# Performance work log

Measured on AMD Instinct MI355X. Metric: run time of the kernel, lower is better.

## Reference

```python
import jax, jax.numpy as jnp
import numpy as np

N_NODES = 50000
N_EDGES = 640000
N_SUPPORT = 3
D_IN = 128
D_OUT = 128


def setup_inputs() -> dict:
    key = jax.random.key(0)
    k = jax.random.split(key, 6)
    x = jax.random.normal(k[0], (N_NODES, D_IN), dtype=jnp.float32)
    edge_rows = jax.random.randint(k[1], (N_SUPPORT, N_EDGES), 0, N_NODES, dtype=jnp.int32)
    edge_cols = jax.random.randint(k[2], (N_SUPPORT, N_EDGES), 0, N_NODES, dtype=jnp.int32)
    edge_vals = jax.random.uniform(k[3], (N_SUPPORT, N_EDGES), dtype=jnp.float32)
    weights = jax.random.normal(k[4], (N_SUPPORT, D_IN, D_OUT), dtype=jnp.float32) * 0.05
    bias = jax.random.normal(k[5], (D_OUT,), dtype=jnp.float32) * 0.01
    return {"x": x, "edge_rows": edge_rows, "edge_cols": edge_cols,
            "edge_vals": edge_vals, "weights": weights, "bias": bias}


def reference(x, edge_rows, edge_cols, edge_vals, weights, bias):
    # Dense projection per support: [S, N, D_OUT]
    pre = jnp.einsum('nd,sdo->sno', x, weights)

    def spmm(rows, cols, vals, dense):
        # sparse [N,N] @ dense [N,D] via gather + scatter-add
        msgs = vals[:, None] * dense[cols]          # [E, D]
        return jax.ops.segment_sum(msgs, rows, num_segments=dense.shape[0])

    out = jax.vmap(spmm)(edge_rows, edge_cols, edge_vals, pre).sum(axis=0)
    return jax.nn.relu(out + bias)
```

## Files before the change

### kernel.cpp

```cpp
#include <hip/hip_runtime.h>

#define N_NODES 50000
#define N_EDGES 640000
#define N_SUP   3
#define D       128
#define NTOT    150000
#define E_TOT   1920000
#define NC      293
#define CAPC    7680
#define CAPB    9216
#define CTILE   2048
#define CTPS    313
#define SBLKS   (N_SUP * CTPS)
#define XCBLKS  3125
#define WBLKS   96
#define LDSTR   132

typedef __attribute__((ext_vector_type(2))) float f32x2;
typedef __attribute__((ext_vector_type(4))) float f32x4;
typedef __attribute__((ext_vector_type(8))) short s16x8;

__device__ __forceinline__ unsigned short f2bf(float f) {
    unsigned int u = __float_as_uint(f);
    u += 0x7FFFu + ((u >> 16) & 1u);
    return (unsigned short)(u >> 16);
}

__global__ __launch_bounds__(512) void prep_scatter(
    const int* __restrict__ rows, const int* __restrict__ cols,
    const float* __restrict__ vals, int* __restrict__ coarse_wptr,
    uint2* __restrict__ sortedA,
    const float4* __restrict__ x, ushort4* __restrict__ xb,
    const float* __restrict__ W, unsigned short* __restrict__ Wf)
{
    int tid = threadIdx.x;

    if (blockIdx.x >= SBLKS) {
        int gid = (blockIdx.x - SBLKS) * 512 + tid;
        if (gid < N_NODES * D / 4) {
            float4 v = x[gid];
            ushort4 o;
            o.x = f2bf(v.x); o.y = f2bf(v.y); o.z = f2bf(v.z); o.w = f2bf(v.w);
            xb[gid] = o;
        } else {
            int g2 = gid - N_NODES * D / 4;
            if (g2 < N_SUP * D * D) {
                int j    = g2 & 7;
                int lane = (g2 >> 3) & 63;
                int rest = g2 >> 9;
                int nt = rest & 7, kb = (rest >> 3) & 3, s = rest >> 5;
                int k = kb * 32 + ((lane >> 4) * 8) + j;
                int n = nt * 16 + (lane & 15);
                Wf[g2] = f2bf(W[((size_t)s * D + k) * D + n]);
            }
        }
        return;
    }

    __shared__ int          h[512];
    __shared__ int          toff[512];
    __shared__ int          gbase[512];
    __shared__ uint2        stage[CTILE];
    __shared__ unsigned int dst[CTILE];

    h[tid] = 0;
    __syncthreads();

    int s  = blockIdx.x / CTPS;
    int tb = (blockIdx.x % CTPS) * CTILE;
    int n  = N_EDGES - tb; if (n > CTILE) n = CTILE;
    const int*   rp = rows + (size_t)s * N_EDGES + tb;
    const int*   cp = cols + (size_t)s * N_EDGES + tb;
    const float* vp = vals + (size_t)s * N_EDGES + tb;

    int bk[4], rk[4]; uint2 ed[4];
    #pragma unroll
    for (int i = 0; i < 4; ++i) {
        int idx = tid + i * 512;
        bk[i] = -1;
        if (idx < n) {
            int grow = s * N_NODES + rp[idx];
            bk[i] = grow >> 9;
            rk[i] = atomicAdd(&h[bk[i]], 1);
            ed[i] = make_uint2(((unsigned int)(grow & 511) << 16)
                               | (unsigned int)cp[idx],
                               __float_as_uint(vp[idx]));
        }
    }
    __syncthreads();
    int cntb = h[tid];
    __syncthreads();
    for (int off = 1; off < 512; off <<= 1) {
        int t = (tid >= off) ? h[tid - off] : 0;
        __syncthreads();
        h[tid] += t;
        __syncthreads();
    }
    toff[tid]  = h[tid] - cntb;
    gbase[tid] = (cntb > 0) ? atomicAdd(&coarse_wptr[tid], cntb) : 0;
    __syncthreads();

    #pragma unroll
    for (int i = 0; i < 4; ++i) {
        if (bk[i] >= 0) {
            int slot = toff[bk[i]] + rk[i];
            int gslot = gbase[bk[i]] + rk[i];
            stage[slot] = ed[i];
            dst[slot] = (gslot < CAPC)
                      ? (unsigned int)(bk[i] * CAPC + gslot)
                      : 0xFFFFFFFFu;
        }
    }
    __syncthreads();
    for (int j = tid; j < n; j += 512) {
        unsigned int d = dst[j];
        if (d != 0xFFFFFFFFu) sortedA[d] = stage[j];
    }
}

__global__ __launch_bounds__(512) void bucket_sort(
    const int* __restrict__ coarse_wptr, const uint2* __restrict__ sortedA,
    int* __restrict__ row_ptr2, unsigned int* __restrict__ sortedB)
{
    int c  = blockIdx.x;
    int cnt = coarse_wptr[c];
    if (cnt > CAPC) cnt = CAPC;

    __shared__ int hist[512];
    __shared__ int rank[512];
    __shared__ int fin[512];
    int tid = threadIdx.x;
    hist[tid] = 0;

    const uint2* src = sortedA + (size_t)c * CAPC;
    uint2 e[15];
    #pragma unroll
    for (int k = 0; k < 15; ++k) {
        int idx = tid + k * 512;
        if (idx < cnt) e[k] = src[idx];
    }
    __syncthreads();
    #pragma unroll
    for (int k = 0; k < 15; ++k) {
        int idx = tid + k * 512;
        if (idx < cnt) atomicAdd(&hist[e[k].x >> 16], 1);
    }
    __syncthreads();

    int padded = (hist[tid] + 3) & ~3;
    hist[tid] = padded;
    __syncthreads();
    for (int off = 1; off < 512; off <<= 1) {
        int t = (tid >= off) ? hist[tid - off] : 0;
        __syncthreads();
        hist[tid] += t;
        __syncthreads();
    }
    int start = c * CAPB + hist[tid] - padded;
    rank[tid] = start;
    fin [tid] = start + padded;
    row_ptr2[c * 513 + tid] = start;
    if (tid == 511) row_ptr2[c * 513 + 512] = c * CAPB + hist[511];
    __syncthreads();

    #pragma unroll
    for (int k = 0; k < 15; ++k) {
        int idx = tid + k * 512;
        if (idx < cnt) {
            int r = atomicAdd(&rank[e[k].x >> 16], 1);
            sortedB[r] = ((unsigned int)f2bf(__uint_as_float(e[k].y)) << 16)
                       | (e[k].x & 0xFFFFu);
        }
    }
    __syncthreads();
    for (int p = rank[tid]; p < fin[tid]; ++p) sortedB[p] = 0;
}

__global__ __launch_bounds__(256) void gather_gemm(
    const unsigned short* __restrict__ xb, const int* __restrict__ row_ptr2,
    const unsigned int* __restrict__ sortedB,
    const unsigned short* __restrict__ Wf,
    const float* __restrict__ bias, float* __restrict__ out)
{
    __shared__ unsigned short ys[48 * LDSTR];
    __shared__ int rs[48], re[48];
    const int tid  = threadIdx.x;
    const int w    = tid >> 6;
    const int lane = tid & 63;
    const int m0   = blockIdx.x * 16;

    if (tid < 48) {
        int grow = (tid >> 4) * N_NODES + m0 + (tid & 15);
        int rpi  = (grow >> 9) * 513 + (grow & 511);
        rs[tid] = row_ptr2[rpi];
        re[tid] = row_ptr2[rpi + 1];
    }
    __syncthreads();

    const int hh = lane >> 5;
    const int u  = lane & 31;
    for (int r = w; r < 48; r += 4) {
        int start = rs[r], end = re[r];
        f32x2 accA = {0.f, 0.f}, accB = {0.f, 0.f};
        for (int j = start; j < end; j += 64) {
            int m = end - j; if (m > 64) m = 64;
            unsigned int ev = (lane < m) ? sortedB[j + lane] : 0u;
            for (int t = 0; t < m; t += 4) {
                unsigned int e0 = (unsigned int)__shfl((int)ev, t + hh);
                unsigned int e1 = (unsigned int)__shfl((int)ev, t + 2 + hh);
                float v0 = __uint_as_float(e0 & 0xFFFF0000u);
                float v1 = __uint_as_float(e1 & 0xFFFF0000u);
                uint2 X0 = *((const uint2*)(xb + (size_t)(e0 & 0xFFFFu) * D) + u);
                uint2 X1 = *((const uint2*)(xb + (size_t)(e1 & 0xFFFFu) * D) + u);
                f32x2 xa0 = {__uint_as_float(X0.x << 16),
                             __uint_as_float(X0.x & 0xFFFF0000u)};
                f32x2 xb0 = {__uint_as_float(X0.y << 16),
                             __uint_as_float(X0.y & 0xFFFF0000u)};
                f32x2 xa1 = {__uint_as_float(X1.x << 16),
                             __uint_as_float(X1.x & 0xFFFF0000u)};
                f32x2 xb1 = {__uint_as_float(X1.y << 16),
                             __uint_as_float(X1.y & 0xFFFF0000u)};
                accA += v0 * xa0;
                accB += v0 * xb0;
                accA += v1 * xa1;
                accB += v1 * xb1;
            }
        }
        float a0 = accA.x, a1 = accA.y, a2 = accB.x, a3 = accB.y;
        a0 += __shfl_xor(a0, 32);
        a1 += __shfl_xor(a1, 32);
        a2 += __shfl_xor(a2, 32);
        a3 += __shfl_xor(a3, 32);
        if (hh == 0) {
            uint2 o;
            o.x = (unsigned int)f2bf(a0) | ((unsigned int)f2bf(a1) << 16);
            o.y = (unsigned int)f2bf(a2) | ((unsigned int)f2bf(a3) << 16);
            *(uint2*)(ys + r * LDSTR + u * 4) = o;
        }
    }
    __syncthreads();

    const int quad = lane >> 4;
    const int l16  = lane & 15;
    const int nt0  = w * 2;
    f32x4 acc0 = {0.f, 0.f, 0.f, 0.f}, acc1 = {0.f, 0.f, 0.f, 0.f};

    #pragma unroll
    for (int s = 0; s < N_SUP; ++s) {
        #pragma unroll
        for (int kb = 0; kb < 4; ++kb) {
            union { uint2 q[2]; s16x8 v; } A;
            const unsigned short* ap = ys + (s * 16 + l16) * LDSTR
                                          + kb * 32 + quad * 8;
            A.q[0] = *(const uint2*)ap;
            A.q[1] = *(const uint2*)(ap + 4);
            const unsigned short* wf = Wf + (size_t)((s * 4 + kb) * 8 + nt0) * 64 * 8
                                          + lane * 8;
            s16x8 b0 = *(const s16x8*)wf;
            s16x8 b1 = *(const s16x8*)(wf + 64 * 8);
            acc0 = __builtin_amdgcn_mfma_f32_16x16x32_bf16(A.v, b0, acc0, 0, 0, 0);
            acc1 = __builtin_amdgcn_mfma_f32_16x16x32_bf16(A.v, b1, acc1, 0, 0, 0);
        }
    }

    #pragma unroll
    for (int p = 0; p < 2; ++p) {
        int col = (nt0 + p) * 16 + l16;
        float bv = bias[col];
        f32x4 a = p ? acc1 : acc0;
        #pragma unroll
        for (int r = 0; r < 4; ++r) {
            int row = m0 + quad * 4 + r;
            out[(size_t)row * D + col] = fmaxf(a[r] + bv, 0.f);
        }
    }
}

extern "C" void kernel_launch(void* const* d_in, const int* in_sizes, int n_in,
                              void* d_out, int out_size, void* d_ws, size_t ws_size,
                              hipStream_t stream)
{
    const float* x         = (const float*)d_in[0];
    const int*   edge_rows = (const int*)  d_in[1];
    const int*   edge_cols = (const int*)  d_in[2];
    const float* edge_vals = (const float*)d_in[3];
    const float* weights   = (const float*)d_in[4];
    const float* bias      = (const float*)d_in[5];
    float* out = (float*)d_out;

    char* ws = (char*)d_ws;
    size_t off = 0;
    auto alloc = [&](size_t bytes) -> char* {
        char* p = ws + off;
        off += (bytes + 255) & ~(size_t)255;
        return p;
    };
    int*            coarse_wptr = (int*)            alloc(512 * 4);
    int*            row_ptr2    = (int*)            alloc((size_t)NC * 513 * 4);
    unsigned short* xb          = (unsigned short*) alloc((size_t)N_NODES * D * 2);
    unsigned short* Wf          = (unsigned short*) alloc((size_t)N_SUP * D * D * 2);
    uint2*          sortedA     = (uint2*)          alloc((size_t)NC * CAPC * 8);
    unsigned int*   sortedB     = (unsigned int*)   alloc((size_t)NC * CAPB * 4);

    hipMemsetAsync(coarse_wptr, 0, 512 * 4, stream);
    prep_scatter<<<SBLKS + XCBLKS + WBLKS, 512, 0, stream>>>(
        edge_rows, edge_cols, edge_vals, coarse_wptr, sortedA,
        (const float4*)x, (ushort4*)xb, weights, Wf);
    bucket_sort <<<NC, 512, 0, stream>>>(coarse_wptr, sortedA,
                                         row_ptr2, sortedB);
    gather_gemm <<<N_NODES / 16, 256, 0, stream>>>(xb, row_ptr2, sortedB,
                                                   Wf, bias, out);
}
```

Measured before the change: 197.7 us.

## Build CSR with global count, scan and atomic placement instead of bucket sort

Replaces the two-level sort (coarse LDS-staged scatter into buckets, then a per-bucket sort) with three passes. The first counts edges per row with global atomics, fused with the bf16 conversion of x and W. The second scans the counts per 512-row chunk, and the third places each edge directly into its slot with a global atomic on a per-row write pointer. This removes the intermediate sortedA buffer and its write and read traffic. In exchange it issues two global atomics per edge, writes scattered 4-byte entries, and drops the padding of row lengths to multiples of four that the gather kernel may have relied on.

Measured after the change: 378.7 us. 91.6% more time.

```diff
diff --git a/kernel.cpp b/kernel.cpp
--- a/kernel.cpp
+++ b/kernel.cpp
@@ -7,11 +7,8 @@
 #define NTOT    150000
 #define E_TOT   1920000
 #define NC      293
-#define CAPC    7680
 #define CAPB    9216
-#define CTILE   2048
-#define CTPS    313
-#define SBLKS   (N_SUP * CTPS)
+#define CBLKS   938
 #define XCBLKS  3125
 #define WBLKS   96
 #define LDSTR   132
@@ -26,154 +23,93 @@
     return (unsigned short)(u >> 16);
 }
 
-__global__ __launch_bounds__(512) void prep_scatter(
-    const int* __restrict__ rows, const int* __restrict__ cols,
-    const float* __restrict__ vals, int* __restrict__ coarse_wptr,
-    uint2* __restrict__ sortedA,
+__global__ __launch_bounds__(512) void count_convert(
+    const int* __restrict__ rows, int* __restrict__ row_cnt,
     const float4* __restrict__ x, ushort4* __restrict__ xb,
     const float* __restrict__ W, unsigned short* __restrict__ Wf)
 {
     int tid = threadIdx.x;
 
-    if (blockIdx.x >= SBLKS) {
-        int gid = (blockIdx.x - SBLKS) * 512 + tid;
-        if (gid < N_NODES * D / 4) {
-            float4 v = x[gid];
-            ushort4 o;
-            o.x = f2bf(v.x); o.y = f2bf(v.y); o.z = f2bf(v.z); o.w = f2bf(v.w);
-            xb[gid] = o;
-        } else {
-            int g2 = gid - N_NODES * D / 4;
-            if (g2 < N_SUP * D * D) {
-                int j    = g2 & 7;
-                int lane = (g2 >> 3) & 63;
-                int rest = g2 >> 9;
-                int nt = rest & 7, kb = (rest >> 3) & 3, s = rest >> 5;
-                int k = kb * 32 + ((lane >> 4) * 8) + j;
-                int n = nt * 16 + (lane & 15);
-                Wf[g2] = f2bf(W[((size_t)s * D + k) * D + n]);
+    if (blockIdx.x < CBLKS) {
+        int base = blockIdx.x * 2048 + tid;
+        #pragma unroll
+        for (int i = 0; i < 4; ++i) {
+            int idx = base + i * 512;
+            if (idx < E_TOT) {
+                int s = idx / N_EDGES;
+                atomicAdd(&row_cnt[s * N_NODES + rows[idx]], 1);
             }
         }
         return;
     }
 
-    __shared__ int          h[512];
-    __shared__ int          toff[512];
-    __shared__ int          gbase[512];
-    __shared__ uint2        stage[CTILE];
-    __shared__ unsigned int dst[CTILE];
-
-    h[tid] = 0;
+    int gid = (blockIdx.x - CBLKS) * 512 + tid;
+    if (gid < N_NODES * D / 4) {
+        float4 v = x[gid];
+        ushort4 o;
+        o.x = f2bf(v.x); o.y = f2bf(v.y); o.z = f2bf(v.z); o.w = f2bf(v.w);
+        xb[gid] = o;
+    } else {
+        int g2 = gid - N_NODES * D / 4;
+        if (g2 < N_SUP * D * D) {
+            int j    = g2 & 7;
+            int lane = (g2 >> 3) & 63;
+            int rest = g2 >> 9;
+            int nt = rest & 7, kb = (rest >> 3) & 3, s = rest >> 5;
+            int k = kb * 32 + ((lane >> 4) * 8) + j;
+            int n = nt * 16 + (lane & 15);
+            Wf[g2] = f2bf(W[((size_t)s * D + k) * D + n]);
+        }
+    }
+}
+
+__global__ __launch_bounds__(512) void scan_rows(
+    const int* __restrict__ row_cnt, int* __restrict__ row_ptr2,
+    int* __restrict__ row_wptr)
+{
+    __shared__ int wsum[8];
+    int c    = blockIdx.x;
+    int tid  = threadIdx.x;
+    int lane = tid & 63;
+    int w    = tid >> 6;
+    int grow = c * 512 + tid;
+    int cnt  = (grow < NTOT) ? row_cnt[grow] : 0;
+
+    int v = cnt;
+    #pragma unroll
+    for (int d = 1; d < 64; d <<= 1) {
+        int t = __shfl_up(v, d);
+        v += (lane >= d) ? t : 0;
+    }
+    if (lane == 63) wsum[w] = v;
     __syncthreads();
-
-    int s  = blockIdx.x / CTPS;
-    int tb = (blockIdx.x % CTPS) * CTILE;
-    int n  = N_EDGES - tb; if (n > CTILE) n = CTILE;
-    const int*   rp = rows + (size_t)s * N_EDGES + tb;
-    const int*   cp = cols + (size_t)s * N_EDGES + tb;
-    const float* vp = vals + (size_t)s * N_EDGES + tb;
-
-    int bk[4], rk[4]; uint2 ed[4];
+    int base = c * CAPB;
+    #pragma unroll
+    for (int i = 0; i < 8; ++i) base += (i < w) ? wsum[i] : 0;
+
+    int start = base + v - cnt;
+    row_ptr2[c * 513 + tid] = start;
+    if (grow < NTOT) row_wptr[grow] = start;
+    if (tid == 511) row_ptr2[c * 513 + 512] = base + v;
+}
+
+__global__ __launch_bounds__(512) void place(
+    const int* __restrict__ rows, const int* __restrict__ cols,
+    const float* __restrict__ vals, int* __restrict__ row_wptr,
+    unsigned int* __restrict__ sortedB)
+{
+    int base = blockIdx.x * 2048 + threadIdx.x;
     #pragma unroll
     for (int i = 0; i < 4; ++i) {
-        int idx = tid + i * 512;
-        bk[i] = -1;
-        if (idx < n) {
-            int grow = s * N_NODES + rp[idx];
-            bk[i] = grow >> 9;
-            rk[i] = atomicAdd(&h[bk[i]], 1);
-            ed[i] = make_uint2(((unsigned int)(grow & 511) << 16)
-                               | (unsigned int)cp[idx],
-                               __float_as_uint(vp[idx]));
-        }
-    }
-    __syncthreads();
-    int cntb = h[tid];
-    __syncthreads();
-    for (int off = 1; off < 512; off <<= 1) {
-        int t = (tid >= off) ? h[tid - off] : 0;
-        __syncthreads();
-        h[tid] += t;
-        __syncthreads();
-    }
-    toff[tid]  = h[tid] - cntb;
-    gbase[tid] = (cntb > 0) ? atomicAdd(&coarse_wptr[tid], cntb) : 0;
-    __syncthreads();
-
-    #pragma unroll
-    for (int i = 0; i < 4; ++i) {
-        if (bk[i] >= 0) {
-            int slot = toff[bk[i]] + rk[i];
-            int gslot = gbase[bk[i]] + rk[i];
-            stage[slot] = ed[i];
-            dst[slot] = (gslot < CAPC)
-                      ? (unsigned int)(bk[i] * CAPC + gslot)
-                      : 0xFFFFFFFFu;
-        }
-    }
-    __syncthreads();
-    for (int j = tid; j < n; j += 512) {
-        unsigned int d = dst[j];
-        if (d != 0xFFFFFFFFu) sortedA[d] = stage[j];
-    }
-}
-
-__global__ __launch_bounds__(512) void bucket_sort(
-    const int* __restrict__ coarse_wptr, const uint2* __restrict__ sortedA,
-    int* __restrict__ row_ptr2, unsigned int* __restrict__ sortedB)
-{
-    int c  = blockIdx.x;
-    int cnt = coarse_wptr[c];
-    if (cnt > CAPC) cnt = CAPC;
-
-    __shared__ int hist[512];
-    __shared__ int rank[512];
-    __shared__ int fin[512];
-    int tid = threadIdx.x;
-    hist[tid] = 0;
-
-    const uint2* src = sortedA + (size_t)c * CAPC;
-    uint2 e[15];
-    #pragma unroll
-    for (int k = 0; k < 15; ++k) {
-        int idx = tid + k * 512;
-        if (idx < cnt) e[k] = src[idx];
-    }
-    __syncthreads();
-    #pragma unroll
-    for (int k = 0; k < 15; ++k) {
-        int idx = tid + k * 512;
-        if (idx < cnt) atomicAdd(&hist[e[k].x >> 16], 1);
-    }
-    __syncthreads();
-
-    int padded = (hist[tid] + 3) & ~3;
-    hist[tid] = padded;
-    __syncthreads();
-    for (int off = 1; off < 512; off <<= 1) {
-        int t = (tid >= off) ? hist[tid - off] : 0;
-        __syncthreads();
-        hist[tid] += t;
-        __syncthreads();
-    }
-    int start = c * CAPB + hist[tid] - padded;
-    rank[tid] = start;
-    fin [tid] = start + padded;
-    row_ptr2[c * 513 + tid] = start;
-    if (tid == 511) row_ptr2[c * 513 + 512] = c * CAPB + hist[511];
-    __syncthreads();
-
-    #pragma unroll
-    for (int k = 0; k < 15; ++k) {
-        int idx = tid + k * 512;
-        if (idx < cnt) {
-            int r = atomicAdd(&rank[e[k].x >> 16], 1);
-            sortedB[r] = ((unsigned int)f2bf(__uint_as_float(e[k].y)) << 16)
-                       | (e[k].x & 0xFFFFu);
-        }
-    }
-    __syncthreads();
-    for (int p = rank[tid]; p < fin[tid]; ++p) sortedB[p] = 0;
+        int idx = base + i * 512;
+        if (idx < E_TOT) {
+            int s    = idx / N_EDGES;
+            int grow = s * N_NODES + rows[idx];
+            int pos  = atomicAdd(&row_wptr[grow], 1);
+            sortedB[pos] = ((unsigned int)f2bf(vals[idx]) << 16)
+                         | (unsigned int)cols[idx];
+        }
+    }
 }
 
 __global__ __launch_bounds__(256) void gather_gemm(
@@ -295,19 +231,19 @@
         off += (bytes + 255) & ~(size_t)255;
         return p;
     };
-    int*            coarse_wptr = (int*)            alloc(512 * 4);
-    int*            row_ptr2    = (int*)            alloc((size_t)NC * 513 * 4);
-    unsigned short* xb          = (unsigned short*) alloc((size_t)N_NODES * D * 2);
-    unsigned short* Wf          = (unsigned short*) alloc((size_t)N_SUP * D * D * 2);
-    uint2*          sortedA     = (uint2*)          alloc((size_t)NC * CAPC * 8);
-    unsigned int*   sortedB     = (unsigned int*)   alloc((size_t)NC * CAPB * 4);
-
-    hipMemsetAsync(coarse_wptr, 0, 512 * 4, stream);
-    prep_scatter<<<SBLKS + XCBLKS + WBLKS, 512, 0, stream>>>(
-        edge_rows, edge_cols, edge_vals, coarse_wptr, sortedA,
-        (const float4*)x, (ushort4*)xb, weights, Wf);
-    bucket_sort <<<NC, 512, 0, stream>>>(coarse_wptr, sortedA,
-                                         row_ptr2, sortedB);
-    gather_gemm <<<N_NODES / 16, 256, 0, stream>>>(xb, row_ptr2, sortedB,
-                                                   Wf, bias, out);
-}
+    int*            row_cnt  = (int*)            alloc((size_t)NTOT * 4);
+    int*            row_wptr = (int*)            alloc((size_t)NTOT * 4);
+    int*            row_ptr2 = (int*)            alloc((size_t)NC * 513 * 4);
+    unsigned short* xb       = (unsigned short*) alloc((size_t)N_NODES * D * 2);
+    unsigned short* Wf       = (unsigned short*) alloc((size_t)N_SUP * D * D * 2);
+    unsigned int*   sortedB  = (unsigned int*)   alloc((size_t)(NC + 1) * CAPB * 4);
+
+    hipMemsetAsync(row_cnt, 0, (size_t)NTOT * 4, stream);
+    count_convert<<<CBLKS + XCBLKS + WBLKS, 512, 0, stream>>>(
+        edge_rows, row_cnt, (const float4*)x, (ushort4*)xb, weights, Wf);
+    scan_rows<<<NC, 512, 0, stream>>>(row_cnt, row_ptr2, row_wptr);
+    place<<<CBLKS, 512, 0, stream>>>(edge_rows, edge_cols, edge_vals,
+                                     row_wptr, sortedB);
+    gather_gemm<<<N_NODES / 16, 256, 0, stream>>>(xb, row_ptr2, sortedB,
+                                                  Wf, bias, out);
+}
```

## Split edge staging into packed key and bf16 value arrays, use wave-shuffle scans

Applied to the files above, without the earlier changes.

Edges in the intermediate coarse-bucket buffer are now stored as a 4-byte packed row/col key plus a 2-byte bf16 value, instead of an 8-byte uint2 with an fp32 value. The bf16 conversion moves into the first pass, which cuts intermediate write and read bytes. Both LDS Hillis-Steele prefix scans are replaced with a wave-level __shfl_up scan plus a cross-wave sum, removing many __syncthreads. The global bucket counters are spaced 16 ints apart to reduce atomic contention. Per-row padding to a multiple of 4 and its zero-fill are dropped (CAPB becomes CAPC). That is a risk if gather_gemm assumes rows padded to 4 entries.

Result: no change. 199.1 us (+0.7%).

```diff
diff --git a/kernel.cpp b/kernel.cpp
--- a/kernel.cpp
+++ b/kernel.cpp
@@ -8,7 +8,6 @@
 #define E_TOT   1920000
 #define NC      293
 #define CAPC    7680
-#define CAPB    9216
 #define CTILE   2048
 #define CTPS    313
 #define SBLKS   (N_SUP * CTPS)
@@ -29,7 +28,7 @@
 __global__ __launch_bounds__(512) void prep_scatter(
     const int* __restrict__ rows, const int* __restrict__ cols,
     const float* __restrict__ vals, int* __restrict__ coarse_wptr,
-    uint2* __restrict__ sortedA,
+    unsigned int* __restrict__ sortedM, unsigned short* __restrict__ sortedV,
     const float4* __restrict__ x, ushort4* __restrict__ xb,
     const float* __restrict__ W, unsigned short* __restrict__ Wf)
 {
@@ -57,11 +56,16 @@
         return;
     }
 
-    __shared__ int          h[512];
-    __shared__ int          toff[512];
-    __shared__ int          gbase[512];
-    __shared__ uint2        stage[CTILE];
-    __shared__ unsigned int dst[CTILE];
+    __shared__ int            h[512];
+    __shared__ int            toff[512];
+    __shared__ int            gbase[512];
+    __shared__ int            wsum[8];
+    __shared__ unsigned int   stageM[CTILE];
+    __shared__ unsigned short stageV[CTILE];
+    __shared__ unsigned int   dst[CTILE];
+
+    const int lane = tid & 63;
+    const int w    = tid >> 6;
 
     h[tid] = 0;
     __syncthreads();
@@ -73,7 +77,7 @@
     const int*   cp = cols + (size_t)s * N_EDGES + tb;
     const float* vp = vals + (size_t)s * N_EDGES + tb;
 
-    int bk[4], rk[4]; uint2 ed[4];
+    int bk[4], rk[4]; unsigned int edM[4]; unsigned short edV[4];
     #pragma unroll
     for (int i = 0; i < 4; ++i) {
         int idx = tid + i * 512;
@@ -82,30 +86,37 @@
             int grow = s * N_NODES + rp[idx];
             bk[i] = grow >> 9;
             rk[i] = atomicAdd(&h[bk[i]], 1);
-            ed[i] = make_uint2(((unsigned int)(grow & 511) << 16)
-                               | (unsigned int)cp[idx],
-                               __float_as_uint(vp[idx]));
+            edM[i] = ((unsigned int)(grow & 511) << 16) | (unsigned int)cp[idx];
+            edV[i] = f2bf(vp[idx]);
         }
     }
     __syncthreads();
     int cntb = h[tid];
-    __syncthreads();
-    for (int off = 1; off < 512; off <<= 1) {
-        int t = (tid >= off) ? h[tid - off] : 0;
-        __syncthreads();
-        h[tid] += t;
-        __syncthreads();
-    }
-    toff[tid]  = h[tid] - cntb;
-    gbase[tid] = (cntb > 0) ? atomicAdd(&coarse_wptr[tid], cntb) : 0;
+
+    int v = cntb;
+    #pragma unroll
+    for (int d = 1; d < 64; d <<= 1) {
+        int t = __shfl_up(v, d);
+        v += (lane >= d) ? t : 0;
+    }
+    if (lane == 63) wsum[w] = v;
+    __syncthreads();
+    int add = 0;
+    #pragma unroll
+    for (int i = 0; i < 8; ++i) add += (i < w) ? wsum[i] : 0;
+    int incl = v + add;
+
+    toff[tid]  = incl - cntb;
+    gbase[tid] = (cntb > 0) ? atomicAdd(&coarse_wptr[tid * 16], cntb) : 0;
     __syncthreads();
 
     #pragma unroll
     for (int i = 0; i < 4; ++i) {
         if (bk[i] >= 0) {
-            int slot = toff[bk[i]] + rk[i];
+            int slot  = toff[bk[i]] + rk[i];
             int gslot = gbase[bk[i]] + rk[i];
-            stage[slot] = ed[i];
+            stageM[slot] = edM[i];
+            stageV[slot] = edV[i];
             dst[slot] = (gslot < CAPC)
                       ? (unsigned int)(bk[i] * CAPC + gslot)
                       : 0xFFFFFFFFu;
@@ -114,66 +125,76 @@
     __syncthreads();
     for (int j = tid; j < n; j += 512) {
         unsigned int d = dst[j];
-        if (d != 0xFFFFFFFFu) sortedA[d] = stage[j];
+        if (d != 0xFFFFFFFFu) {
+            sortedM[d] = stageM[j];
+            sortedV[d] = stageV[j];
+        }
     }
 }
 
 __global__ __launch_bounds__(512) void bucket_sort(
-    const int* __restrict__ coarse_wptr, const uint2* __restrict__ sortedA,
+    const int* __restrict__ coarse_wptr,
+    const unsigned int* __restrict__ sortedM,
+    const unsigned short* __restrict__ sortedV,
     int* __restrict__ row_ptr2, unsigned int* __restrict__ sortedB)
 {
-    int c  = blockIdx.x;
-    int cnt = coarse_wptr[c];
+    int c   = blockIdx.x;
+    int cnt = coarse_wptr[c * 16];
     if (cnt > CAPC) cnt = CAPC;
 
     __shared__ int hist[512];
     __shared__ int rank[512];
-    __shared__ int fin[512];
-    int tid = threadIdx.x;
+    __shared__ int wsum[8];
+    int tid  = threadIdx.x;
+    int lane = tid & 63;
+    int w    = tid >> 6;
     hist[tid] = 0;
 
-    const uint2* src = sortedA + (size_t)c * CAPC;
-    uint2 e[15];
+    const unsigned int*   srcM = sortedM + (size_t)c * CAPC;
+    const unsigned short* srcV = sortedV + (size_t)c * CAPC;
+    unsigned int   m[15];
+    unsigned short vv[15];
     #pragma unroll
     for (int k = 0; k < 15; ++k) {
         int idx = tid + k * 512;
-        if (idx < cnt) e[k] = src[idx];
+        if (idx < cnt) { m[k] = srcM[idx]; vv[k] = srcV[idx]; }
     }
     __syncthreads();
     #pragma unroll
     for (int k = 0; k < 15; ++k) {
         int idx = tid + k * 512;
-        if (idx < cnt) atomicAdd(&hist[e[k].x >> 16], 1);
-    }
-    __syncthreads();
-
-    int padded = (hist[tid] + 3) & ~3;
-    hist[tid] = padded;
-    __syncthreads();
-    for (int off = 1; off < 512; off <<= 1) {
-        int t = (tid >= off) ? hist[tid - off] : 0;
-        __syncthreads();
-        hist[tid] += t;
-        __syncthreads();
-    }
-    int start = c * CAPB + hist[tid] - padded;
+        if (idx < cnt) atomicAdd(&hist[m[k] >> 16], 1);
+    }
+    __syncthreads();
+
+    int cntb = hist[tid];
+    int v = cntb;
+    #pragma unroll
+    for (int d = 1; d < 64; d <<= 1) {
+        int t = __shfl_up(v, d);
+        v += (lane >= d) ? t : 0;
+    }
+    if (lane == 63) wsum[w] = v;
+    __syncthreads();
+    int add = 0;
+    #pragma unroll
+    for (int i = 0; i < 8; ++i) add += (i < w) ? wsum[i] : 0;
+    int incl = v + add;
+
+    int start = c * CAPC + incl - cntb;
     rank[tid] = start;
-    fin [tid] = start + padded;
     row_ptr2[c * 513 + tid] = start;
-    if (tid == 511) row_ptr2[c * 513 + 512] = c * CAPB + hist[511];
+    if (tid == 511) row_ptr2[c * 513 + 512] = c * CAPC + incl;
     __syncthreads();
 
     #pragma unroll
     for (int k = 0; k < 15; ++k) {
         int idx = tid + k * 512;
         if (idx < cnt) {
-            int r = atomicAdd(&rank[e[k].x >> 16], 1);
-            sortedB[r] = ((unsigned int)f2bf(__uint_as_float(e[k].y)) << 16)
-                       | (e[k].x & 0xFFFFu);
-        }
-    }
-    __syncthreads();
-    for (int p = rank[tid]; p < fin[tid]; ++p) sortedB[p] = 0;
+            int r = atomicAdd(&rank[m[k] >> 16], 1);
+            sortedB[r] = ((unsigned int)vv[k] << 16) | (m[k] & 0xFFFFu);
+        }
+    }
 }
 
 __global__ __launch_bounds__(256) void gather_gemm(
@@ -295,19 +316,20 @@
         off += (bytes + 255) & ~(size_t)255;
         return p;
     };
-    int*            coarse_wptr = (int*)            alloc(512 * 4);
+    int*            coarse_wptr = (int*)            alloc(512 * 16 * 4);
     int*            row_ptr2    = (int*)            alloc((size_t)NC * 513 * 4);
     unsigned short* xb          = (unsigned short*) alloc((size_t)N_NODES * D * 2);
     unsigned short* Wf          = (unsigned short*) alloc((size_t)N_SUP * D * D * 2);
-    uint2*          sortedA     = (uint2*)          alloc((size_t)NC * CAPC * 8);
-    unsigned int*   sortedB     = (unsigned int*)   alloc((size_t)NC * CAPB * 4);
-
-    hipMemsetAsync(coarse_wptr, 0, 512 * 4, stream);
+    unsigned int*   sortedM     = (unsigned int*)   alloc((size_t)NC * CAPC * 4);
+    unsigned short* sortedV     = (unsigned short*) alloc((size_t)NC * CAPC * 2);
+    unsigned int*   sortedB     = (unsigned int*)   alloc((size_t)NC * CAPC * 4);
+
+    hipMemsetAsync(coarse_wptr, 0, 512 * 16 * 4, stream);
     prep_scatter<<<SBLKS + XCBLKS + WBLKS, 512, 0, stream>>>(
-        edge_rows, edge_cols, edge_vals, coarse_wptr, sortedA,
+        edge_rows, edge_cols, edge_vals, coarse_wptr, sortedM, sortedV,
         (const float4*)x, (ushort4*)xb, weights, Wf);
-    bucket_sort <<<NC, 512, 0, stream>>>(coarse_wptr, sortedA,
+    bucket_sort <<<NC, 512, 0, stream>>>(coarse_wptr, sortedM, sortedV,
                                          row_ptr2, sortedB);
-    gather_gemm <<<N_NODES / 16, 256, 0, stream>>>(xb, row_ptr2, sortedB,
-                                                   Wf, bias, out);
-}
+    gather_gemm<<<N_NODES / 16, 256, 0, stream>>>(xb, row_ptr2, sortedB,
+                                                  Wf, bias, out);
+}
```
